# Performance work log

Hardware: AMD Instinct MI355X
Metric: run time of the kernel (lower is better)

## Reference

```python
import jax, jax.numpy as jnp
import numpy as np

WS = 7            # window_size
N = WS * WS       # 49 tokens per window
C = 192           # embed_dims
H = 6             # num_heads
HD = C // H       # head_dim = 32
D = 2             # depth
F = 768           # feedforward_channels
BW = 8192         # nW * B


def _rel_index():
    # Swin relative position index for a WSxWS window -> [N, N] int
    coords = np.stack(np.meshgrid(np.arange(WS), np.arange(WS), indexing='ij')).reshape(2, -1)
    rel = coords[:, :, None] - coords[:, None, :]           # [2, N, N]
    rel = rel.transpose(1, 2, 0).astype(np.int64)           # [N, N, 2]
    rel[..., 0] += WS - 1
    rel[..., 1] += WS - 1
    rel[..., 0] *= 2 * WS - 1
    return rel.sum(-1)                                      # [N, N]


def _ln(x, w, b, eps=1e-5):
    mu = jnp.mean(x, axis=-1, keepdims=True)
    var = jnp.var(x, axis=-1, keepdims=True)
    return (x - mu) * jax.lax.rsqrt(var + eps) * w + b


def setup_inputs() -> dict:
    key = jax.random.key(0)
    ks = jax.random.split(key, 8)
    s = 0.02
    return {
        'x': jax.random.normal(ks[0], (BW, N, C), dtype=jnp.float32),
        'window_indices': jnp.zeros((BW,), dtype=jnp.int32),
        'norm1_w': jnp.ones((D, C), jnp.float32),
        'norm1_b': jnp.zeros((D, C), jnp.float32),
        'qkv_w': jax.random.normal(ks[1], (D, 3 * C, C), dtype=jnp.float32) * s,
        'qkv_b': jnp.zeros((D, 3 * C), jnp.float32),
        'rel_bias': jax.random.normal(ks[2], (D, (2 * WS - 1) ** 2, H), dtype=jnp.float32) * s,
        'proj_w': jax.random.normal(ks[3], (D, C, C), dtype=jnp.float32) * s,
        'proj_b': jnp.zeros((D, C), jnp.float32),
        'norm2_w': jnp.ones((D, C), jnp.float32),
        'norm2_b': jnp.zeros((D, C), jnp.float32),
        'ffn_w1': jax.random.normal(ks[4], (D, F, C), dtype=jnp.float32) * s,
        'ffn_b1': jnp.zeros((D, F), jnp.float32),
        'ffn_w2': jax.random.normal(ks[5], (D, C, F), dtype=jnp.float32) * s,
        'ffn_b2': jnp.zeros((D, C), jnp.float32),
    }


def reference(x, window_indices, norm1_w, norm1_b, qkv_w, qkv_b, rel_bias,
              proj_w, proj_b, norm2_w, norm2_b, ffn_w1, ffn_b1, ffn_w2, ffn_b2):
    ridx = jnp.asarray(_rel_index())   # [N, N]
    scale = HD ** -0.5
    for i in range(D):
        # --- windowed MSA block ---
        identity = x
        h = _ln(x, norm1_w[i], norm1_b[i])
        qkv = h @ qkv_w[i].T + qkv_b[i]                      # [BW, N, 3C]
        qkv = qkv.reshape(BW, N, 3, H, HD).transpose(2, 0, 3, 1, 4)
        q, k, v = qkv[0] * scale, qkv[1], qkv[2]             # [BW, H, N, HD]
        attn = jnp.einsum('bhqd,bhkd->bhqk', q, k)           # [BW, H, N, N]
        bias = rel_bias[i][ridx].transpose(2, 0, 1)          # [H, N, N]
        attn = jax.nn.softmax(attn + bias[None], axis=-1)
        o = jnp.einsum('bhqk,bhkd->bhqd', attn, v)           # [BW, H, N, HD]
        o = o.transpose(0, 2, 1, 3).reshape(BW, N, C)
        o = o @ proj_w[i].T + proj_b[i]
        x = o + identity
        # --- FFN block ---
        identity = x
        h = _ln(x, norm2_w[i], norm2_b[i])
        h = jax.nn.gelu(h @ ffn_w1[i].T + ffn_b1[i], approximate=False)
        x = h @ ffn_w2[i].T + ffn_b2[i] + identity
    # heightmerging is None -> window_indices unused
    return x
```

## Files before the change

### kernel.cpp

```cpp
#include <hip/hip_runtime.h>
#include <math.h>

typedef short s16;
typedef __attribute__((ext_vector_type(8))) short short8;
typedef __attribute__((ext_vector_type(4))) float f32x4;

#define NTOK 49
#define CDIM 192
#define NH   6
#define HDIM 32
#define FFD  768
#define QSCALE 0.17677669529663687f

__device__ __forceinline__ s16 f2bf(float f) {
    union { float f; unsigned u; } v; v.f = f;
    unsigned r = v.u + 0x7fffu + ((v.u >> 16) & 1u);
    return (s16)(r >> 16);
}

__global__ void prep_weights(const float* __restrict__ qkv_w,
                             const float* __restrict__ proj_w,
                             const float* __restrict__ w1,
                             const float* __restrict__ w2,
                             s16* __restrict__ wb) {
    int idx = blockIdx.x * 256 + threadIdx.x;
    if (idx < 221184)       wb[idx] = f2bf(qkv_w[idx]);
    else if (idx < 294912)  wb[idx] = f2bf(proj_w[idx - 221184]);
    else if (idx < 589824)  wb[idx] = f2bf(w1[idx - 294912]);
    else if (idx < 884736)  wb[idx] = f2bf(w2[idx - 589824]);
}

__global__ void prep_bias(const float* __restrict__ rel_bias, float* __restrict__ bias_pad) {
    int idx = blockIdx.x * 256 + threadIdx.x;
    if (idx >= 2 * NH * NTOK * 64) return;
    int k = idx & 63;
    int q = (idx >> 6) % NTOK;
    int h = ((idx >> 6) / NTOK) % NH;
    int d = idx / (64 * NTOK * NH);
    float v;
    if (k < NTOK) {
        int qi = q / 7, qj = q % 7, ki = k / 7, kj = k % 7;
        int r = (qi - ki + 6) * 13 + (qj - kj + 6);
        v = rel_bias[(d * 169 + r) * NH + h];
    } else {
        v = -1e9f;
    }
    bias_pad[idx] = v;
}

__global__ __launch_bounds__(256, 1)
void swin_fused(const float* __restrict__ x_in,
                const float* __restrict__ n1w, const float* __restrict__ n1b,
                const s16*  __restrict__ qkv_wb, const float* __restrict__ qkv_b,
                const float* __restrict__ bias_pad,
                const s16*  __restrict__ proj_wb, const float* __restrict__ proj_b,
                const float* __restrict__ n2w, const float* __restrict__ n2b,
                const s16*  __restrict__ w1b, const float* __restrict__ fb1,
                const s16*  __restrict__ w2b, const float* __restrict__ fb2,
                float* __restrict__ out)
{
    __shared__ float xb[NTOK][196];
    __shared__ s16   hb[64][200];
    __shared__ __align__(16) char ubuf[77824];
    __shared__ s16   sb[64][72];
    s16 (*qk)[392] = (s16(*)[392])ubuf;
    s16 *vt        = (s16*)(ubuf + 50176);
    s16 (*tb)[392] = (s16(*)[392])ubuf;

    const int tid  = threadIdx.x;
    const int wv   = tid >> 6;
    const int lane = tid & 63;
    const int lr   = lane & 15;
    const int lg   = lane >> 4;
    const int win  = blockIdx.x;

    {
        const float4* xg = (const float4*)(x_in + (size_t)win * (NTOK * CDIM));
        for (int idx = tid; idx < NTOK * CDIM / 4; idx += 256) {
            float4 v = xg[idx];
            int n = (idx * 4) / CDIM, c = (idx * 4) % CDIM;
            xb[n][c] = v.x; xb[n][c + 1] = v.y; xb[n][c + 2] = v.z; xb[n][c + 3] = v.w;
        }
        for (int idx = tid; idx < 15 * 200; idx += 256)
            hb[NTOK + idx / 200][idx % 200] = 0;
    }
    __syncthreads();

    for (int blk = 0; blk < 2; ++blk) {
        const s16* qw  = qkv_wb + (size_t)blk * (3 * CDIM * CDIM);
        const s16* pw  = proj_wb + (size_t)blk * (CDIM * CDIM);
        const s16* f1w = w1b + (size_t)blk * (FFD * CDIM);
        const s16* f2w = w2b + (size_t)blk * (CDIM * FFD);

        if (tid < 196) {
            int r = tid >> 2, q4 = tid & 3;
            float s = 0.f, s2 = 0.f;
            for (int c = q4; c < CDIM; c += 4) { float v = xb[r][c]; s += v; s2 += v * v; }
            s  += __shfl_xor(s, 1);  s  += __shfl_xor(s, 2);
            s2 += __shfl_xor(s2, 1); s2 += __shfl_xor(s2, 2);
            float mu = s * (1.f / CDIM);
            float rs = rsqrtf(s2 * (1.f / CDIM) - mu * mu + 1e-5f);
            for (int c = q4; c < CDIM; c += 4)
                hb[r][c] = f2bf((xb[r][c] - mu) * rs * n1w[blk * CDIM + c] + n1b[blk * CDIM + c]);
        }
        __syncthreads();

        {
            short8 Af[4][6];
            #pragma unroll
            for (int m = 0; m < 4; ++m)
                #pragma unroll
                for (int k = 0; k < 6; ++k)
                    Af[m][k] = *(const short8*)&hb[m * 16 + lr][k * 32 + lg * 8];

            const int ct0 = wv * 9, ct1 = ct0 + 9;
            short8 Bf[6], Bn[6];
            {
                const s16* p = qw + (size_t)(ct0 * 16 + lr) * CDIM + lg * 8;
                #pragma unroll
                for (int k = 0; k < 6; ++k) Bf[k] = *(const short8*)(p + k * 32);
            }
            for (int ct = ct0; ct < ct1; ++ct) {
                if (ct + 1 < ct1) {
                    const s16* p = qw + (size_t)((ct + 1) * 16 + lr) * CDIM + lg * 8;
                    #pragma unroll
                    for (int k = 0; k < 6; ++k) Bn[k] = *(const short8*)(p + k * 32);
                }
                f32x4 acc[4];
                #pragma unroll
                for (int m = 0; m < 4; ++m) { f32x4 z = {0.f, 0.f, 0.f, 0.f}; acc[m] = z; }
                #pragma unroll
                for (int k = 0; k < 6; ++k)
                    #pragma unroll
                    for (int m = 0; m < 4; ++m)
                        acc[m] = __builtin_amdgcn_mfma_f32_16x16x32_bf16(Af[m][k], Bf[k], acc[m], 0, 0, 0);
                const int c = ct * 16 + lr;
                const float bias = qkv_b[blk * 3 * CDIM + c];
                #pragma unroll
                for (int m = 0; m < 4; ++m)
                    #pragma unroll
                    for (int j = 0; j < 4; ++j) {
                        int row = m * 16 + lg * 4 + j;
                        float v = acc[m][j] + bias;
                        if (c < 384) {
                            if (c < 192) v *= QSCALE;
                            qk[row][c] = f2bf(v);
                        } else {
                            vt[(c - 384) * 72 + row] = f2bf(v);
                        }
                    }
                if (ct + 1 < ct1) {
                    #pragma unroll
                    for (int k = 0; k < 6; ++k) Bf[k] = Bn[k];
                }
            }
        }
        __syncthreads();

        {
            const int m = wv;
            for (int h = 0; h < NH; ++h) {
                short8 Aq = *(const short8*)&qk[m * 16 + lr][h * HDIM + lg * 8];
                f32x4 sc[4];
                #pragma unroll
                for (int ct = 0; ct < 4; ++ct) {
                    short8 Bk = *(const short8*)&qk[ct * 16 + lr][CDIM + h * HDIM + lg * 8];
                    f32x4 z = {0.f, 0.f, 0.f, 0.f};
                    sc[ct] = __builtin_amdgcn_mfma_f32_16x16x32_bf16(Aq, Bk, z, 0, 0, 0);
                }
                const float* bp = bias_pad + (size_t)(blk * NH + h) * NTOK * 64;
                float inv[4];
                #pragma unroll
                for (int j = 0; j < 4; ++j) {
                    int q = m * 16 + lg * 4 + j;
                    float v0 = sc[0][j], v1 = sc[1][j], v2 = sc[2][j], v3 = sc[3][j];
                    if (q < NTOK) {
                        const float* bq = bp + q * 64 + lr;
                        v0 += bq[0]; v1 += bq[16]; v2 += bq[32]; v3 += bq[48];
                    }
                    float mx = fmaxf(fmaxf(v0, v1), fmaxf(v2, v3));
                    #pragma unroll
                    for (int msk = 1; msk < 16; msk <<= 1) mx = fmaxf(mx, __shfl_xor(mx, msk));
                    v0 = __expf(v0 - mx); v1 = __expf(v1 - mx);
                    v2 = __expf(v2 - mx); v3 = __expf(v3 - mx);
                    float sum = v0 + v1 + v2 + v3;
                    #pragma unroll
                    for (int msk = 1; msk < 16; msk <<= 1) sum += __shfl_xor(sum, msk);
                    inv[j] = 1.f / sum;
                    int row = m * 16 + lg * 4 + j;
                    sb[row][lr]      = f2bf(v0);
                    sb[row][16 + lr] = f2bf(v1);
                    sb[row][32 + lr] = f2bf(v2);
                    sb[row][48 + lr] = f2bf(v3);
                }
                short8 Ap0 = *(const short8*)&sb[m * 16 + lr][lg * 8];
                short8 Ap1 = *(const short8*)&sb[m * 16 + lr][32 + lg * 8];
                #pragma unroll
                for (int cb = 0; cb < 2; ++cb) {
                    const s16* vrow = vt + (size_t)(h * HDIM + cb * 16 + lr) * 72;
                    short8 Bv0 = *(const short8*)(vrow + lg * 8);
                    short8 Bv1 = *(const short8*)(vrow + 32 + lg * 8);
                    f32x4 z = {0.f, 0.f, 0.f, 0.f};
                    f32x4 o = __builtin_amdgcn_mfma_f32_16x16x32_bf16(Ap0, Bv0, z, 0, 0, 0);
                    o = __builtin_amdgcn_mfma_f32_16x16x32_bf16(Ap1, Bv1, o, 0, 0, 0);
                    #pragma unroll
                    for (int j = 0; j < 4; ++j) {
                        int row = m * 16 + lg * 4 + j;
                        if (row < NTOK) hb[row][h * HDIM + cb * 16 + lr] = f2bf(o[j] * inv[j]);
                    }
                }
            }
        }
        __syncthreads();

        {
            short8 Af[4][6];
            #pragma unroll
            for (int m = 0; m < 4; ++m)
                #pragma unroll
                for (int k = 0; k < 6; ++k)
                    Af[m][k] = *(const short8*)&hb[m * 16 + lr][k * 32 + lg * 8];

            const int ct0 = wv * 3, ct1 = ct0 + 3;
            short8 Bf[6], Bn[6];
            {
                const s16* p = pw + (size_t)(ct0 * 16 + lr) * CDIM + lg * 8;
                #pragma unroll
                for (int k = 0; k < 6; ++k) Bf[k] = *(const short8*)(p + k * 32);
            }
            for (int ct = ct0; ct < ct1; ++ct) {
                if (ct + 1 < ct1) {
                    const s16* p = pw + (size_t)((ct + 1) * 16 + lr) * CDIM + lg * 8;
                    #pragma unroll
                    for (int k = 0; k < 6; ++k) Bn[k] = *(const short8*)(p + k * 32);
                }
                f32x4 acc[4];
                #pragma unroll
                for (int m = 0; m < 4; ++m) { f32x4 z = {0.f, 0.f, 0.f, 0.f}; acc[m] = z; }
                #pragma unroll
                for (int k = 0; k < 6; ++k)
                    #pragma unroll
                    for (int m = 0; m < 4; ++m)
                        acc[m] = __builtin_amdgcn_mfma_f32_16x16x32_bf16(Af[m][k], Bf[k], acc[m], 0, 0, 0);
                const int c = ct * 16 + lr;
                const float bias = proj_b[blk * CDIM + c];
                #pragma unroll
                for (int m = 0; m < 4; ++m)
                    #pragma unroll
                    for (int j = 0; j < 4; ++j) {
                        int row = m * 16 + lg * 4 + j;
                        if (row < NTOK) xb[row][c] = acc[m][j] + bias + xb[row][c];
                    }
                if (ct + 1 < ct1) {
                    #pragma unroll
                    for (int k = 0; k < 6; ++k) Bf[k] = Bn[k];
                }
            }
        }
        __syncthreads();

        if (tid < 196) {
            int r = tid >> 2, q4 = tid & 3;
            float s = 0.f, s2 = 0.f;
            for (int c = q4; c < CDIM; c += 4) { float v = xb[r][c]; s += v; s2 += v * v; }
            s  += __shfl_xor(s, 1);  s  += __shfl_xor(s, 2);
            s2 += __shfl_xor(s2, 1); s2 += __shfl_xor(s2, 2);
            float mu = s * (1.f / CDIM);
            float rs = rsqrtf(s2 * (1.f / CDIM) - mu * mu + 1e-5f);
            for (int c = q4; c < CDIM; c += 4)
                hb[r][c] = f2bf((xb[r][c] - mu) * rs * n2w[blk * CDIM + c] + n2b[blk * CDIM + c]);
        }
        __syncthreads();

        {
            f32x4 acc2[3][4];
            #pragma unroll
            for (int cc = 0; cc < 3; ++cc)
                #pragma unroll
                for (int m = 0; m < 4; ++m) { f32x4 z = {0.f, 0.f, 0.f, 0.f}; acc2[cc][m] = z; }

            for (int ch = 0; ch < 2; ++ch) {
                {
                    short8 Af[4][6];
                    #pragma unroll
                    for (int m = 0; m < 4; ++m)
                        #pragma unroll
                        for (int k = 0; k < 6; ++k)
                            Af[m][k] = *(const short8*)&hb[m * 16 + lr][k * 32 + lg * 8];

                    const int ct0 = wv * 6, ct1 = ct0 + 6;
                    short8 Bf[6], Bn[6];
                    {
                        const s16* p = f1w + (size_t)(ch * 384 + ct0 * 16 + lr) * CDIM + lg * 8;
                        #pragma unroll
                        for (int k = 0; k < 6; ++k) Bf[k] = *(const short8*)(p + k * 32);
                    }
                    for (int ct = ct0; ct < ct1; ++ct) {
                        if (ct + 1 < ct1) {
                            const s16* p = f1w + (size_t)(ch * 384 + (ct + 1) * 16 + lr) * CDIM + lg * 8;
                            #pragma unroll
                            for (int k = 0; k < 6; ++k) Bn[k] = *(const short8*)(p + k * 32);
                        }
                        f32x4 acc[4];
                        #pragma unroll
                        for (int m = 0; m < 4; ++m) { f32x4 z = {0.f, 0.f, 0.f, 0.f}; acc[m] = z; }
                        #pragma unroll
                        for (int k = 0; k < 6; ++k)
                            #pragma unroll
                            for (int m = 0; m < 4; ++m)
                                acc[m] = __builtin_amdgcn_mfma_f32_16x16x32_bf16(Af[m][k], Bf[k], acc[m], 0, 0, 0);
                        const int cl = ct * 16 + lr;
                        const float bias = fb1[blk * FFD + ch * 384 + cl];
                        #pragma unroll
                        for (int m = 0; m < 4; ++m)
                            #pragma unroll
                            for (int j = 0; j < 4; ++j) {
                                int row = m * 16 + lg * 4 + j;
                                float v = acc[m][j] + bias;
                                v = 0.5f * v * (1.f + erff(v * 0.70710678118654752f));
                                tb[row][cl] = f2bf(v);
                            }
                        if (ct + 1 < ct1) {
                            #pragma unroll
                            for (int k = 0; k < 6; ++k) Bf[k] = Bn[k];
                        }
                    }
                }
                __syncthreads();
                {
                    const int c0t = wv * 3;
                    short8 B2[3], B2n[3], A2[4];
                    #pragma unroll
                    for (int cc = 0; cc < 3; ++cc) {
                        int c = (c0t + cc) * 16 + lr;
                        B2[cc] = *(const short8*)(f2w + (size_t)c * FFD + ch * 384 + lg * 8);
                    }
                    for (int kt = 0; kt < 12; ++kt) {
                        if (kt < 11) {
                            #pragma unroll
                            for (int cc = 0; cc < 3; ++cc) {
                                int c = (c0t + cc) * 16 + lr;
                                B2n[cc] = *(const short8*)(f2w + (size_t)c * FFD + ch * 384 + (kt + 1) * 32 + lg * 8);
                            }
                        }
                        #pragma unroll
                        for (int m = 0; m < 4; ++m)
                            A2[m] = *(const short8*)&tb[m * 16 + lr][kt * 32 + lg * 8];
                        #pragma unroll
                        for (int cc = 0; cc < 3; ++cc)
                            #pragma unroll
                            for (int m = 0; m < 4; ++m)
                                acc2[cc][m] = __builtin_amdgcn_mfma_f32_16x16x32_bf16(A2[m], B2[cc], acc2[cc][m], 0, 0, 0);
                        if (kt < 11) {
                            #pragma unroll
                            for (int cc = 0; cc < 3; ++cc) B2[cc] = B2n[cc];
                        }
                    }
                }
                __syncthreads();
            }
            #pragma unroll
            for (int cc = 0; cc < 3; ++cc) {
                const int c = (wv * 3 + cc) * 16 + lr;
                const float bias = fb2[blk * CDIM + c];
                #pragma unroll
                for (int m = 0; m < 4; ++m)
                    #pragma unroll
                    for (int j = 0; j < 4; ++j) {
                        int row = m * 16 + lg * 4 + j;
                        if (row < NTOK) xb[row][c] = acc2[cc][m][j] + bias + xb[row][c];
                    }
            }
        }
        __syncthreads();
    }

    {
        float* ow = out + (size_t)win * (NTOK * CDIM);
        for (int idx = tid; idx < NTOK * CDIM / 4; idx += 256) {
            int n = (idx * 4) / CDIM, c = (idx * 4) % CDIM;
            float4 v = make_float4(xb[n][c], xb[n][c + 1], xb[n][c + 2], xb[n][c + 3]);
            ((float4*)ow)[idx] = v;
        }
    }
}

extern "C" void kernel_launch(void* const* d_in, const int* in_sizes, int n_in,
                              void* d_out, int out_size, void* d_ws, size_t ws_size,
                              hipStream_t stream) {
    const float* x      = (const float*)d_in[0];
    const float* n1w    = (const float*)d_in[2];
    const float* n1b    = (const float*)d_in[3];
    const float* qkv_w  = (const float*)d_in[4];
    const float* qkv_b  = (const float*)d_in[5];
    const float* rel    = (const float*)d_in[6];
    const float* proj_w = (const float*)d_in[7];
    const float* proj_b = (const float*)d_in[8];
    const float* n2w    = (const float*)d_in[9];
    const float* n2b    = (const float*)d_in[10];
    const float* w1     = (const float*)d_in[11];
    const float* b1     = (const float*)d_in[12];
    const float* w2     = (const float*)d_in[13];
    const float* b2     = (const float*)d_in[14];

    s16*   wb   = (s16*)d_ws;
    float* bpad = (float*)((char*)d_ws + 884736 * 2);

    prep_weights<<<3456, 256, 0, stream>>>(qkv_w, proj_w, w1, w2, wb);
    prep_bias<<<147, 256, 0, stream>>>(rel, bpad);

    const s16* qkv_wb  = wb;
    const s16* proj_wb = wb + 221184;
    const s16* w1b     = wb + 294912;
    const s16* w2b     = wb + 589824;

    swin_fused<<<8192, 256, 0, stream>>>(x, n1w, n1b, qkv_wb, qkv_b, bpad,
                                         proj_wb, proj_b, n2w, n2b,
                                         w1b, b1, w2b, b2, (float*)d_out);
}
```

Baseline: 4.710 ms.

## Use 512-thread blocks splitting row tiles across waves, and switch GELU to tanh form

Doubles the threads per window from 256 to 512. Each of the 8 waves now handles two of the four 16-row M tiles and a quarter of the output column tiles, and attention splits the heads between two wave groups with a double-buffered score scratch. LayerNorm uses 8 lanes per row. The aim is more waves in flight per CU to hide memory and MFMA latency. The tradeoff is that each B weight fragment loaded from global memory now feeds only two M tiles instead of four, so weight traffic per window doubles. The exact erf GELU is also replaced by a tanh approximation built from exp, which diverges slightly from the reference's exact GELU.

```diff
diff --git a/kernel.cpp b/kernel.cpp
--- a/kernel.cpp
+++ b/kernel.cpp
@@ -16,6 +16,13 @@
     union { float f; unsigned u; } v; v.f = f;
     unsigned r = v.u + 0x7fffu + ((v.u >> 16) & 1u);
     return (s16)(r >> 16);
+}
+
+__device__ __forceinline__ float gelu_f(float x) {
+    float y = 1.5957691216057308f * (x + 0.044715f * x * x * x);
+    float e = __expf(y);
+    float t = 1.f - 2.f / (e + 1.f);
+    return 0.5f * x * (1.f + t);
 }
 
 __global__ void prep_weights(const float* __restrict__ qkv_w,
@@ -48,7 +55,7 @@
     bias_pad[idx] = v;
 }
 
-__global__ __launch_bounds__(256, 1)
+__global__ __launch_bounds__(512, 2)
 void swin_fused(const float* __restrict__ x_in,
                 const float* __restrict__ n1w, const float* __restrict__ n1b,
                 const s16*  __restrict__ qkv_wb, const float* __restrict__ qkv_b,
@@ -59,10 +66,10 @@
                 const s16*  __restrict__ w2b, const float* __restrict__ fb2,
                 float* __restrict__ out)
 {
-    __shared__ float xb[NTOK][196];
+    __shared__ float xb[NTOK][194];
     __shared__ s16   hb[64][200];
     __shared__ __align__(16) char ubuf[77824];
-    __shared__ s16   sb[64][72];
+    __shared__ s16   sb[2][64][72];
     s16 (*qk)[392] = (s16(*)[392])ubuf;
     s16 *vt        = (s16*)(ubuf + 50176);
     s16 (*tb)[392] = (s16(*)[392])ubuf;
@@ -72,16 +79,18 @@
     const int lane = tid & 63;
     const int lr   = lane & 15;
     const int lg   = lane >> 4;
+    const int mt0  = (wv >> 2) * 2;
+    const int cq   = wv & 3;
     const int win  = blockIdx.x;
 
     {
         const float4* xg = (const float4*)(x_in + (size_t)win * (NTOK * CDIM));
-        for (int idx = tid; idx < NTOK * CDIM / 4; idx += 256) {
+        for (int idx = tid; idx < NTOK * CDIM / 4; idx += 512) {
             float4 v = xg[idx];
             int n = (idx * 4) / CDIM, c = (idx * 4) % CDIM;
             xb[n][c] = v.x; xb[n][c + 1] = v.y; xb[n][c + 2] = v.z; xb[n][c + 3] = v.w;
         }
-        for (int idx = tid; idx < 15 * 200; idx += 256)
+        for (int idx = tid; idx < 15 * 200; idx += 512)
             hb[NTOK + idx / 200][idx % 200] = 0;
     }
     __syncthreads();
@@ -92,28 +101,28 @@
         const s16* f1w = w1b + (size_t)blk * (FFD * CDIM);
         const s16* f2w = w2b + (size_t)blk * (CDIM * FFD);
 
-        if (tid < 196) {
-            int r = tid >> 2, q4 = tid & 3;
+        if (tid < 392) {
+            int r = tid >> 3, q8 = tid & 7;
             float s = 0.f, s2 = 0.f;
-            for (int c = q4; c < CDIM; c += 4) { float v = xb[r][c]; s += v; s2 += v * v; }
-            s  += __shfl_xor(s, 1);  s  += __shfl_xor(s, 2);
-            s2 += __shfl_xor(s2, 1); s2 += __shfl_xor(s2, 2);
+            for (int c = q8; c < CDIM; c += 8) { float v = xb[r][c]; s += v; s2 += v * v; }
+            s  += __shfl_xor(s, 1);  s  += __shfl_xor(s, 2);  s  += __shfl_xor(s, 4);
+            s2 += __shfl_xor(s2, 1); s2 += __shfl_xor(s2, 2); s2 += __shfl_xor(s2, 4);
             float mu = s * (1.f / CDIM);
             float rs = rsqrtf(s2 * (1.f / CDIM) - mu * mu + 1e-5f);
-            for (int c = q4; c < CDIM; c += 4)
+            for (int c = q8; c < CDIM; c += 8)
                 hb[r][c] = f2bf((xb[r][c] - mu) * rs * n1w[blk * CDIM + c] + n1b[blk * CDIM + c]);
         }
         __syncthreads();
 
         {
-            short8 Af[4][6];
+            short8 Af[2][6];
             #pragma unroll
-            for (int m = 0; m < 4; ++m)
+            for (int m = 0; m < 2; ++m)
                 #pragma unroll
                 for (int k = 0; k < 6; ++k)
-                    Af[m][k] = *(const short8*)&hb[m * 16 + lr][k * 32 + lg * 8];
-
-            const int ct0 = wv * 9, ct1 = ct0 + 9;
+                    Af[m][k] = *(const short8*)&hb[(mt0 + m) * 16 + lr][k * 32 + lg * 8];
+
+            const int ct0 = cq * 9, ct1 = ct0 + 9;
             short8 Bf[6], Bn[6];
             {
                 const s16* p = qw + (size_t)(ct0 * 16 + lr) * CDIM + lg * 8;
@@ -126,21 +135,21 @@
                     #pragma unroll
                     for (int k = 0; k < 6; ++k) Bn[k] = *(const short8*)(p + k * 32);
                 }
-                f32x4 acc[4];
-                #pragma unroll
-                for (int m = 0; m < 4; ++m) { f32x4 z = {0.f, 0.f, 0.f, 0.f}; acc[m] = z; }
+                f32x4 acc[2];
+                #pragma unroll
+                for (int m = 0; m < 2; ++m) { f32x4 z = {0.f, 0.f, 0.f, 0.f}; acc[m] = z; }
                 #pragma unroll
                 for (int k = 0; k < 6; ++k)
                     #pragma unroll
-                    for (int m = 0; m < 4; ++m)
+                    for (int m = 0; m < 2; ++m)
                         acc[m] = __builtin_amdgcn_mfma_f32_16x16x32_bf16(Af[m][k], Bf[k], acc[m], 0, 0, 0);
                 const int c = ct * 16 + lr;
                 const float bias = qkv_b[blk * 3 * CDIM + c];
                 #pragma unroll
-                for (int m = 0; m < 4; ++m)
+                for (int m = 0; m < 2; ++m)
                     #pragma unroll
                     for (int j = 0; j < 4; ++j) {
-                        int row = m * 16 + lg * 4 + j;
+                        int row = (mt0 + m) * 16 + lg * 4 + j;
                         float v = acc[m][j] + bias;
                         if (c < 384) {
                             if (c < 192) v *= QSCALE;
@@ -158,8 +167,10 @@
         __syncthreads();
 
         {
-            const int m = wv;
-            for (int h = 0; h < NH; ++h) {
+            const int m = wv & 3;
+            const int hg = wv >> 2;
+            for (int hh = 0; hh < 3; ++hh) {
+                const int h = hg * 3 + hh;
                 short8 Aq = *(const short8*)&qk[m * 16 + lr][h * HDIM + lg * 8];
                 f32x4 sc[4];
                 #pragma unroll
@@ -188,13 +199,13 @@
                     for (int msk = 1; msk < 16; msk <<= 1) sum += __shfl_xor(sum, msk);
                     inv[j] = 1.f / sum;
                     int row = m * 16 + lg * 4 + j;
-                    sb[row][lr]      = f2bf(v0);
-                    sb[row][16 + lr] = f2bf(v1);
-                    sb[row][32 + lr] = f2bf(v2);
-                    sb[row][48 + lr] = f2bf(v3);
-                }
-                short8 Ap0 = *(const short8*)&sb[m * 16 + lr][lg * 8];
-                short8 Ap1 = *(const short8*)&sb[m * 16 + lr][32 + lg * 8];
+                    sb[hg][row][lr]      = f2bf(v0);
+                    sb[hg][row][16 + lr] = f2bf(v1);
+                    sb[hg][row][32 + lr] = f2bf(v2);
+                    sb[hg][row][48 + lr] = f2bf(v3);
+                }
+                short8 Ap0 = *(const short8*)&sb[hg][m * 16 + lr][lg * 8];
+                short8 Ap1 = *(const short8*)&sb[hg][m * 16 + lr][32 + lg * 8];
                 #pragma unroll
                 for (int cb = 0; cb < 2; ++cb) {
                     const s16* vrow = vt + (size_t)(h * HDIM + cb * 16 + lr) * 72;
@@ -214,14 +225,14 @@
         __syncthreads();
 
         {
-            short8 Af[4][6];
+            short8 Af[2][6];
             #pragma unroll
-            for (int m = 0; m < 4; ++m)
+            for (int m = 0; m < 2; ++m)
                 #pragma unroll
                 for (int k = 0; k < 6; ++k)
-                    Af[m][k] = *(const short8*)&hb[m * 16 + lr][k * 32 + lg * 8];
-
-            const int ct0 = wv * 3, ct1 = ct0 + 3;
+                    Af[m][k] = *(const short8*)&hb[(mt0 + m) * 16 + lr][k * 32 + lg * 8];
+
+            const int ct0 = cq * 3, ct1 = ct0 + 3;
             short8 Bf[6], Bn[6];
             {
                 const s16* p = pw + (size_t)(ct0 * 16 + lr) * CDIM + lg * 8;
@@ -234,21 +245,21 @@
                     #pragma unroll
                     for (int k = 0; k < 6; ++k) Bn[k] = *(const short8*)(p + k * 32);
                 }
-                f32x4 acc[4];
-                #pragma unroll
-                for (int m = 0; m < 4; ++m) { f32x4 z = {0.f, 0.f, 0.f, 0.f}; acc[m] = z; }
+                f32x4 acc[2];
+                #pragma unroll
+                for (int m = 0; m < 2; ++m) { f32x4 z = {0.f, 0.f, 0.f, 0.f}; acc[m] = z; }
                 #pragma unroll
                 for (int k = 0; k < 6; ++k)
                     #pragma unroll
-                    for (int m = 0; m < 4; ++m)
+                    for (int m = 0; m < 2; ++m)
                         acc[m] = __builtin_amdgcn_mfma_f32_16x16x32_bf16(Af[m][k], Bf[k], acc[m], 0, 0, 0);
                 const int c = ct * 16 + lr;
                 const float bias = proj_b[blk * CDIM + c];
                 #pragma unroll
-                for (int m = 0; m < 4; ++m)
+                for (int m = 0; m < 2; ++m)
                     #pragma unroll
                     for (int j = 0; j < 4; ++j) {
-                        int row = m * 16 + lg * 4 + j;
+                        int row = (mt0 + m) * 16 + lg * 4 + j;
                         if (row < NTOK) xb[row][c] = acc[m][j] + bias + xb[row][c];
                     }
                 if (ct + 1 < ct1) {
@@ -259,36 +270,36 @@
         }
         __syncthreads();
 
-        if (tid < 196) {
-            int r = tid >> 2, q4 = tid & 3;
+        if (tid < 392) {
+            int r = tid >> 3, q8 = tid & 7;
             float s = 0.f, s2 = 0.f;
-            for (int c = q4; c < CDIM; c += 4) { float v = xb[r][c]; s += v; s2 += v * v; }
-            s  += __shfl_xor(s, 1);  s  += __shfl_xor(s, 2);
-            s2 += __shfl_xor(s2, 1); s2 += __shfl_xor(s2, 2);
+            for (int c = q8; c < CDIM; c += 8) { float v = xb[r][c]; s += v; s2 += v * v; }
+            s  += __shfl_xor(s, 1);  s  += __shfl_xor(s, 2);  s  += __shfl_xor(s, 4);
+            s2 += __shfl_xor(s2, 1); s2 += __shfl_xor(s2, 2); s2 += __shfl_xor(s2, 4);
             float mu = s * (1.f / CDIM);
             float rs = rsqrtf(s2 * (1.f / CDIM) - mu * mu + 1e-5f);
-            for (int c = q4; c < CDIM; c += 4)
+            for (int c = q8; c < CDIM; c += 8)
                 hb[r][c] = f2bf((xb[r][c] - mu) * rs * n2w[blk * CDIM + c] + n2b[blk * CDIM + c]);
         }
         __syncthreads();
 
         {
-            f32x4 acc2[3][4];
+            f32x4 acc2[3][2];
             #pragma unroll
             for (int cc = 0; cc < 3; ++cc)
                 #pragma unroll
-                for (int m = 0; m < 4; ++m) { f32x4 z = {0.f, 0.f, 0.f, 0.f}; acc2[cc][m] = z; }
+                for (int m = 0; m < 2; ++m) { f32x4 z = {0.f, 0.f, 0.f, 0.f}; acc2[cc][m] = z; }
 
             for (int ch = 0; ch < 2; ++ch) {
                 {
-                    short8 Af[4][6];
-                    #pragma unroll
-                    for (int m = 0; m < 4; ++m)
+                    short8 Af[2][6];
+                    #pragma unroll
+                    for (int m = 0; m < 2; ++m)
                         #pragma unroll
                         for (int k = 0; k < 6; ++k)
-                            Af[m][k] = *(const short8*)&hb[m * 16 + lr][k * 32 + lg * 8];
-
-                    const int ct0 = wv * 6, ct1 = ct0 + 6;
+                            Af[m][k] = *(const short8*)&hb[(mt0 + m) * 16 + lr][k * 32 + lg * 8];
+
+                    const int ct0 = cq * 6, ct1 = ct0 + 6;
                     short8 Bf[6], Bn[6];
                     {
                         const s16* p = f1w + (size_t)(ch * 384 + ct0 * 16 + lr) * CDIM + lg * 8;
@@ -301,24 +312,22 @@
                             #pragma unroll
                             for (int k = 0; k < 6; ++k) Bn[k] = *(const short8*)(p + k * 32);
                         }
-                        f32x4 acc[4];
-                        #pragma unroll
-                        for (int m = 0; m < 4; ++m) { f32x4 z = {0.f, 0.f, 0.f, 0.f}; acc[m] = z; }
+                        f32x4 acc[2];
+                        #pragma unroll
+                        for (int m = 0; m < 2; ++m) { f32x4 z = {0.f, 0.f, 0.f, 0.f}; acc[m] = z; }
                         #pragma unroll
                         for (int k = 0; k < 6; ++k)
                             #pragma unroll
-                            for (int m = 0; m < 4; ++m)
+                            for (int m = 0; m < 2; ++m)
                                 acc[m] = __builtin_amdgcn_mfma_f32_16x16x32_bf16(Af[m][k], Bf[k], acc[m], 0, 0, 0);
                         const int cl = ct * 16 + lr;
                         const float bias = fb1[blk * FFD + ch * 384 + cl];
                         #pragma unroll
-                        for (int m = 0; m < 4; ++m)
+                        for (int m = 0; m < 2; ++m)
                             #pragma unroll
                             for (int j = 0; j < 4; ++j) {
-                                int row = m * 16 + lg * 4 + j;
-                                float v = acc[m][j] + bias;
-                                v = 0.5f * v * (1.f + erff(v * 0.70710678118654752f));
-                                tb[row][cl] = f2bf(v);
+                                int row = (mt0 + m) * 16 + lg * 4 + j;
+                                tb[row][cl] = f2bf(gelu_f(acc[m][j] + bias));
                             }
                         if (ct + 1 < ct1) {
                             #pragma unroll
@@ -328,8 +337,8 @@
                 }
                 __syncthreads();
                 {
-                    const int c0t = wv * 3;
-                    short8 B2[3], B2n[3], A2[4];
+                    const int c0t = cq * 3;
+                    short8 B2[3], B2n[3], A2[2];
                     #pragma unroll
                     for (int cc = 0; cc < 3; ++cc) {
                         int c = (c0t + cc) * 16 + lr;
@@ -344,12 +353,12 @@
                             }
                         }
                         #pragma unroll
-                        for (int m = 0; m < 4; ++m)
-                            A2[m] = *(const short8*)&tb[m * 16 + lr][kt * 32 + lg * 8];
+                        for (int m = 0; m < 2; ++m)
+                            A2[m] = *(const short8*)&tb[(mt0 + m) * 16 + lr][kt * 32 + lg * 8];
                         #pragma unroll
                         for (int cc = 0; cc < 3; ++cc)
                             #pragma unroll
-                            for (int m = 0; m < 4; ++m)
+                            for (int m = 0; m < 2; ++m)
                                 acc2[cc][m] = __builtin_amdgcn_mfma_f32_16x16x32_bf16(A2[m], B2[cc], acc2[cc][m], 0, 0, 0);
                         if (kt < 11) {
                             #pragma unroll
@@ -361,13 +370,13 @@
             }
             #pragma unroll
             for (int cc = 0; cc < 3; ++cc) {
-                const int c = (wv * 3 + cc) * 16 + lr;
+                const int c = (cq * 3 + cc) * 16 + lr;
                 const float bias = fb2[blk * CDIM + c];
                 #pragma unroll
-                for (int m = 0; m < 4; ++m)
+                for (int m = 0; m < 2; ++m)
                     #pragma unroll
                     for (int j = 0; j < 4; ++j) {
-                        int row = m * 16 + lg * 4 + j;
+                        int row = (mt0 + m) * 16 + lg * 4 + j;
                         if (row < NTOK) xb[row][c] = acc2[cc][m][j] + bias + xb[row][c];
                     }
             }
@@ -377,7 +386,7 @@
 
     {
         float* ow = out + (size_t)win * (NTOK * CDIM);
-        for (int idx = tid; idx < NTOK * CDIM / 4; idx += 256) {
+        for (int idx = tid; idx < NTOK * CDIM / 4; idx += 512) {
             int n = (idx * 4) / CDIM, c = (idx * 4) % CDIM;
             float4 v = make_float4(xb[n][c], xb[n][c + 1], xb[n][c + 2], xb[n][c + 3]);
             ((float4*)ow)[idx] = v;
@@ -414,7 +423,7 @@
     const s16* w1b     = wb + 294912;
     const s16* w2b     = wb + 589824;
 
-    swin_fused<<<8192, 256, 0, stream>>>(x, n1w, n1b, qkv_wb, qkv_b, bpad,
+    swin_fused<<<8192, 512, 0, stream>>>(x, n1w, n1b, qkv_wb, qkv_b, bpad,
                                          proj_wb, proj_b, n2w, n2b,
                                          w1b, b1, w2b, b2, (float*)d_out);
 }
```

Result: slower. 5.971 ms (+26.8%).
